# Kernel tuning notes

Hardware: AMD Instinct MI355X
Metric: run time of the kernel (lower is better)

The kernel has to match this reference:

```python
import jax, jax.numpy as jnp
import numpy as np

N = 50000      # nodes
E = 800000     # edges
IN = 30        # atom features
H = 8          # attention heads
D = 32         # per-head out feats
G = 512        # graphs in batch
HID = 128      # predictor hidden
TASKS = 1
ALPHA = 0.2    # LeakyReLU slope
BN_EPS = 1e-5


def setup_inputs() -> dict:
    key = jax.random.key(0)
    ks = jax.random.split(key, 20)
    f = lambda k, shp: (jax.random.normal(k, shp, dtype=jnp.float32) * 0.1)
    return {
        'x': jax.random.normal(ks[0], (N, IN), dtype=jnp.float32),
        'src': jax.random.randint(ks[1], (E,), 0, N, dtype=jnp.int32),
        'dst': jax.random.randint(ks[2], (E,), 0, N, dtype=jnp.int32),
        'graph_ids': jnp.sort(jax.random.randint(ks[3], (N,), 0, G, dtype=jnp.int32)),
        # GAT layer 1 (in=30 -> 8 heads x 32, flatten + ELU, residual projection)
        'W1': f(ks[4], (IN, H * D)),
        'al1': f(ks[5], (H, D)),
        'ar1': f(ks[6], (H, D)),
        'b1': jnp.zeros((H * D,), jnp.float32),
        'resW1': f(ks[7], (IN, H * D)),
        # GAT layer 2 (in=256 -> 8 heads x 32, mean over heads, identity residual)
        'W2': f(ks[8], (H * D, H * D)),
        'al2': f(ks[9], (H, D)),
        'ar2': f(ks[10], (H, D)),
        'b2': jnp.zeros((H * D,), jnp.float32),
        # WeightedSumAndMax readout gate
        'Ww': f(ks[11], (D, 1)),
        'bw': jnp.zeros((1,), jnp.float32),
        # MLP predictor: Linear -> ReLU -> BatchNorm(eval) -> Linear
        'Wp1': f(ks[12], (2 * D, HID)),
        'bp1': jnp.zeros((HID,), jnp.float32),
        'gamma': jnp.ones((HID,), jnp.float32),
        'beta': jnp.zeros((HID,), jnp.float32),
        'rm': jnp.zeros((HID,), jnp.float32),
        'rv': jnp.ones((HID,), jnp.float32),
        'Wp2': f(ks[13], (HID, TASKS)),
        'bp2': jnp.zeros((TASKS,), jnp.float32),
    }


def _gat_layer(h, src, dst, W, al, ar, b):
    # h: [N, F_in] -> out: [N, H, D]
    n = h.shape[0]
    feat = (h @ W).reshape(n, H, D)                    # projected features
    el = jnp.sum(feat * al, axis=-1)                   # [N, H]
    er = jnp.sum(feat * ar, axis=-1)                   # [N, H]
    e = el[src] + er[dst]                              # [E, H]
    e = jnp.where(e > 0, e, ALPHA * e)                 # LeakyReLU
    m = jax.ops.segment_max(e, dst, num_segments=n)    # segment-softmax max
    m = jnp.where(jnp.isfinite(m), m, 0.0)             # guard empty segments
    ex = jnp.exp(e - m[dst])                           # [E, H]
    s = jax.ops.segment_sum(ex, dst, num_segments=n)   # [N, H]
    a = ex / jnp.maximum(s[dst], 1e-9)                 # normalized attention
    msg = a[:, :, None] * feat[src]                    # [E, H, D]
    out = jax.ops.segment_sum(msg, dst, num_segments=n)
    return out + b.reshape(1, H, D)


def reference(x, src, dst, graph_ids, W1, al1, ar1, b1, resW1,
              W2, al2, ar2, b2, Ww, bw, Wp1, bp1, gamma, beta, rm, rv, Wp2, bp2):
    # Layer 1: residual projection (in_feats != H*D), flatten heads, ELU
    h1 = _gat_layer(x, src, dst, W1, al1, ar1, b1)
    h1 = h1 + (x @ resW1).reshape(N, H, D)
    h1 = jax.nn.elu(h1.reshape(N, H * D))
    # Layer 2: identity residual (in_feats == H*D), mean over heads, no activation
    h2 = _gat_layer(h1, src, dst, W2, al2, ar2, b2)
    h2 = h2 + h1.reshape(N, H, D)
    h2 = jnp.mean(h2, axis=1)                          # [N, D]
    # WeightedSumAndMax readout
    w = jax.nn.sigmoid(h2 @ Ww + bw)                   # [N, 1]
    gsum = jax.ops.segment_sum(w * h2, graph_ids, num_segments=G)
    gmax = jax.ops.segment_max(h2, graph_ids, num_segments=G)
    gmax = jnp.where(jnp.isfinite(gmax), gmax, 0.0)
    g = jnp.concatenate([gsum, gmax], axis=-1)         # [G, 2D]
    # MLP predictor (eval-mode BatchNorm)
    p = jax.nn.relu(g @ Wp1 + bp1)
    p = (p - rm) / jnp.sqrt(rv + BN_EPS) * gamma + beta
    return p @ Wp2 + bp2                               # [G, TASKS]
```

## Files before the change

kernel.cpp:

```cpp
#include <hip/hip_runtime.h>
#include <math.h>

#define NN 50000
#define EE 800000
#define IN_F 30
#define NH 8
#define DH 32
#define HD 256
#define NG 512
#define NHID 128
#define ALPHA 0.2f

#define SCAN_B 256
#define SCAN_NB ((NN + SCAN_B - 1)/SCAN_B)

typedef unsigned short u16;

__device__ __forceinline__ u16 f2bf(float f){
  unsigned u = __float_as_uint(f);
  u = u + 0x7FFFu + ((u >> 16) & 1u);
  return (u16)(u >> 16);
}
__device__ __forceinline__ float bf2f(u16 b){
  return __uint_as_float(((unsigned)b) << 16);
}
__device__ __forceinline__ float4 bf4_to_f4(ushort4 v){
  float4 r; r.x=bf2f(v.x); r.y=bf2f(v.y); r.z=bf2f(v.z); r.w=bf2f(v.w); return r;
}

__global__ void k_init(int* counts, int* gcounts){
  int i = blockIdx.x*blockDim.x + threadIdx.x;
  if(i < NN) counts[i] = 0;
  if(i < NG) gcounts[i] = 0;
}

__global__ void k_hist(const int* __restrict__ dst, int* counts){
  int i = blockIdx.x*blockDim.x + threadIdx.x;
  if(i < EE) atomicAdd(&counts[dst[i]], 1);
}

__global__ void k_ghist(const int* __restrict__ gid, int* gcounts){
  int i = blockIdx.x*blockDim.x + threadIdx.x;
  if(i < NN) atomicAdd(&gcounts[gid[i]], 1);
}

__global__ void k_gscan(const int* __restrict__ gcounts, int* __restrict__ gstart){
  __shared__ int sd[NG];
  int t = threadIdx.x;
  int v = gcounts[t];
  sd[t]=v; __syncthreads();
  for(int off=1; off<NG; off<<=1){
    int u = (t>=off)? sd[t-off] : 0;
    __syncthreads();
    sd[t] += u;
    __syncthreads();
  }
  gstart[t] = sd[t]-v;
}

__global__ void k_scan_partial(const int* __restrict__ counts, int* __restrict__ bsums){
  __shared__ int sd[SCAN_B];
  int b = blockIdx.x, t = threadIdx.x;
  int idx = b*SCAN_B + t;
  sd[t] = (idx<NN)? counts[idx] : 0;
  __syncthreads();
  for(int off=SCAN_B/2; off>0; off>>=1){
    if(t<off) sd[t] += sd[t+off];
    __syncthreads();
  }
  if(t==0) bsums[b] = sd[0];
}

__global__ void k_scan_bsums(int* bsums){
  __shared__ int sd[SCAN_B];
  int t = threadIdx.x;
  int v = (t<SCAN_NB)? bsums[t] : 0;
  sd[t]=v; __syncthreads();
  for(int off=1; off<SCAN_B; off<<=1){
    int u = (t>=off)? sd[t-off] : 0;
    __syncthreads();
    sd[t] += u;
    __syncthreads();
  }
  if(t<SCAN_NB) bsums[t] = sd[t]-v;
}

__global__ void k_scan_final(const int* __restrict__ counts, const int* __restrict__ bsums,
                             int* __restrict__ start, int* __restrict__ cursor){
  __shared__ int sd[SCAN_B];
  int b = blockIdx.x, t = threadIdx.x;
  int idx = b*SCAN_B + t;
  int v = (idx<NN)? counts[idx] : 0;
  sd[t]=v; __syncthreads();
  for(int off=1; off<SCAN_B; off<<=1){
    int u = (t>=off)? sd[t-off] : 0;
    __syncthreads();
    sd[t] += u;
    __syncthreads();
  }
  int ex = sd[t]-v + bsums[b];
  if(idx<NN){ start[idx]=ex; cursor[idx]=ex; }
}

__global__ void k_scatter(const int* __restrict__ dst, const int* __restrict__ src,
                          int* cursor, int* __restrict__ csr_src){
  int i = blockIdx.x*blockDim.x + threadIdx.x;
  if(i<EE){ int p = atomicAdd(&cursor[dst[i]],1); csr_src[p]=src[i]; }
}

#define TM1 16
__global__ void k_proj1(const float* __restrict__ x, const float* __restrict__ W1,
                        u16* __restrict__ feat16){
  __shared__ float xs[TM1][IN_F];
  int n0 = blockIdx.x*TM1;
  int t = threadIdx.x;
  for(int i=t;i<TM1*IN_F;i+=256){
    int m=i/IN_F, k=i-m*IN_F;
    xs[m][k] = x[(size_t)(n0+m)*IN_F+k];
  }
  __syncthreads();
  int jq = (t & 63) << 2;
  int m0 = t >> 6;
  float4 acc[4];
  #pragma unroll
  for(int r=0;r<4;r++){ acc[r].x=0.f; acc[r].y=0.f; acc[r].z=0.f; acc[r].w=0.f; }
  for(int k=0;k<IN_F;k++){
    float4 w = *(const float4*)&W1[k*HD + jq];
    #pragma unroll
    for(int r=0;r<4;r++){
      float xv = xs[m0 + (r<<2)][k];
      acc[r].x += xv*w.x; acc[r].y += xv*w.y; acc[r].z += xv*w.z; acc[r].w += xv*w.w;
    }
  }
  #pragma unroll
  for(int r=0;r<4;r++){
    int n = n0 + m0 + (r<<2);
    ushort4 o; o.x=f2bf(acc[r].x); o.y=f2bf(acc[r].y); o.z=f2bf(acc[r].z); o.w=f2bf(acc[r].w);
    *(ushort4*)&feat16[(size_t)n*HD + jq] = o;
  }
}

#define BM 64
#define BN 64
#define BK 16
#define LDP (BM+4)
__global__ void k_proj2(const float* __restrict__ X, const float* __restrict__ W,
                        u16* __restrict__ Y16){
  __shared__ float As[BK][LDP];
  __shared__ float Bs[BK][LDP];
  int t  = threadIdx.x;
  int tx = t & 15, ty = t >> 4;
  int n0 = blockIdx.x*BM;
  int c0 = blockIdx.y*BN;
  float acc[4][4];
  #pragma unroll
  for(int i=0;i<4;i++)
    #pragma unroll
    for(int j=0;j<4;j++) acc[i][j]=0.f;

  int am = t >> 2;
  int ak = (t & 3) << 2;
  int bk = t >> 4;
  int bn = (t & 15) << 2;

  for(int k0=0;k0<HD;k0+=BK){
    int n = n0 + am;
    float4 va = (n<NN) ? *(const float4*)&X[(size_t)n*HD + k0 + ak]
                       : make_float4(0.f,0.f,0.f,0.f);
    float4 vb = *(const float4*)&W[(size_t)(k0+bk)*HD + c0 + bn];
    __syncthreads();
    As[ak+0][am]=va.x; As[ak+1][am]=va.y; As[ak+2][am]=va.z; As[ak+3][am]=va.w;
    *(float4*)&Bs[bk][bn] = vb;
    __syncthreads();
    #pragma unroll
    for(int k=0;k<BK;k++){
      float4 a = *(const float4*)&As[k][ty<<2];
      float4 b = *(const float4*)&Bs[k][tx<<2];
      acc[0][0]+=a.x*b.x; acc[0][1]+=a.x*b.y; acc[0][2]+=a.x*b.z; acc[0][3]+=a.x*b.w;
      acc[1][0]+=a.y*b.x; acc[1][1]+=a.y*b.y; acc[1][2]+=a.y*b.z; acc[1][3]+=a.y*b.w;
      acc[2][0]+=a.z*b.x; acc[2][1]+=a.z*b.y; acc[2][2]+=a.z*b.z; acc[2][3]+=a.z*b.w;
      acc[3][0]+=a.w*b.x; acc[3][1]+=a.w*b.y; acc[3][2]+=a.w*b.z; acc[3][3]+=a.w*b.w;
    }
  }
  #pragma unroll
  for(int i=0;i<4;i++){
    int n = n0 + (ty<<2) + i;
    if(n<NN){
      ushort4 o; o.x=f2bf(acc[i][0]); o.y=f2bf(acc[i][1]); o.z=f2bf(acc[i][2]); o.w=f2bf(acc[i][3]);
      *(ushort4*)&Y16[(size_t)n*HD + c0 + (tx<<2)] = o;
    }
  }
}

__global__ void k_elr(const u16* __restrict__ feat16, const float* __restrict__ al,
                      const float* __restrict__ ar, float* __restrict__ el,
                      float* __restrict__ er){
  int i = blockIdx.x*blockDim.x + threadIdx.x;
  if(i >= NN*NH) return;
  int h = i & 7;
  const ushort4* f4 = (const ushort4*)(feat16 + (size_t)i*DH);
  const float4* a4 = (const float4*)(al + h*DH);
  const float4* b4 = (const float4*)(ar + h*DH);
  float ea=0.f, eb=0.f;
  #pragma unroll
  for(int q=0;q<8;q++){
    float4 f=bf4_to_f4(f4[q]); float4 a=a4[q], b=b4[q];
    ea += f.x*a.x + f.y*a.y + f.z*a.z + f.w*a.w;
    eb += f.x*b.x + f.y*b.y + f.z*b.z + f.w*b.w;
  }
  el[i]=ea; er[i]=eb;
}

__device__ __forceinline__ void gat_agg2(int n, int lane,
    const u16* __restrict__ feat16, const float* __restrict__ el,
    const float* __restrict__ er, const int* __restrict__ start,
    const int* __restrict__ counts, const int* __restrict__ csr_src,
    float* A){
  int half = lane >> 5;
  int l = lane & 31;
  int h = l >> 2;
  int col8 = l << 3;
  float erh = er[n*NH + h];
  int st = start[n], cnt = counts[n];
  float s = 0.f;
  #pragma unroll
  for(int j=0;j<8;j++) A[j]=0.f;
  for(int c=0; c<cnt; c+=64){
    int nrem = cnt - c;
    int lim = nrem < 64 ? nrem : 64;
    int myIdx = csr_src[st + c + (lane < lim ? lane : lim-1)];
    #pragma unroll 4
    for(int k=0; k<lim; k+=2){
      int sel = k + half;
      int sidx = __shfl(myIdx, sel, 64);
      float e = el[(size_t)sidx*NH + h] + erh;
      e = (e>0.f)? e : ALPHA*e;
      float w = (sel < lim) ? __expf(e) : 0.f;
      uint4 rv = *(const uint4*)&feat16[(size_t)sidx*HD + col8];
      float f0 = __uint_as_float(rv.x << 16);
      float f1 = __uint_as_float(rv.x & 0xffff0000u);
      float f2 = __uint_as_float(rv.y << 16);
      float f3 = __uint_as_float(rv.y & 0xffff0000u);
      float f4 = __uint_as_float(rv.z << 16);
      float f5 = __uint_as_float(rv.z & 0xffff0000u);
      float f6 = __uint_as_float(rv.w << 16);
      float f7 = __uint_as_float(rv.w & 0xffff0000u);
      s += w;
      A[0]+=w*f0; A[1]+=w*f1; A[2]+=w*f2; A[3]+=w*f3;
      A[4]+=w*f4; A[5]+=w*f5; A[6]+=w*f6; A[7]+=w*f7;
    }
  }
  s += __shfl_xor(s, 32, 64);
  #pragma unroll
  for(int j=0;j<8;j++) A[j] += __shfl_xor(A[j], 32, 64);
  float inv = 1.f/fmaxf(s, 1e-9f);
  #pragma unroll
  for(int j=0;j<8;j++) A[j] *= inv;
}

__global__ void k_gat1(const u16* __restrict__ feat16, const float* __restrict__ el,
    const float* __restrict__ er, const int* __restrict__ start,
    const int* __restrict__ counts, const int* __restrict__ csr_src,
    const float* __restrict__ x,
    const float* __restrict__ resW1, const float* __restrict__ b1,
    float* __restrict__ h1){
  int n = blockIdx.x*4 + (threadIdx.x>>6);
  int lane = threadIdx.x & 63;
  if(n>=NN) return;
  float A[8];
  gat_agg2(n,lane,feat16,el,er,start,counts,csr_src,A);
  int half = lane>>5, l = lane&31;
  int col8 = l<<3;
  float r[8];
  #pragma unroll
  for(int j=0;j<8;j++) r[j]=0.f;
  const float* xrow = x + (size_t)n*IN_F;
  int kb = half*15;
  #pragma unroll
  for(int k=0;k<15;k++){
    float xv = xrow[kb+k];
    const float4 w0 = *(const float4*)&resW1[(kb+k)*HD + col8];
    const float4 w1 = *(const float4*)&resW1[(kb+k)*HD + col8 + 4];
    r[0]+=xv*w0.x; r[1]+=xv*w0.y; r[2]+=xv*w0.z; r[3]+=xv*w0.w;
    r[4]+=xv*w1.x; r[5]+=xv*w1.y; r[6]+=xv*w1.z; r[7]+=xv*w1.w;
  }
  #pragma unroll
  for(int j=0;j<8;j++) r[j] += __shfl_xor(r[j], 32, 64);
  if(half==0){
    const float4 b0 = *(const float4*)&b1[col8];
    const float4 b4 = *(const float4*)&b1[col8+4];
    float4 o0, o1; float v;
    v = A[0]+r[0]+b0.x; o0.x = (v>0.f)? v : expf(v)-1.f;
    v = A[1]+r[1]+b0.y; o0.y = (v>0.f)? v : expf(v)-1.f;
    v = A[2]+r[2]+b0.z; o0.z = (v>0.f)? v : expf(v)-1.f;
    v = A[3]+r[3]+b0.w; o0.w = (v>0.f)? v : expf(v)-1.f;
    v = A[4]+r[4]+b4.x; o1.x = (v>0.f)? v : expf(v)-1.f;
    v = A[5]+r[5]+b4.y; o1.y = (v>0.f)? v : expf(v)-1.f;
    v = A[6]+r[6]+b4.z; o1.z = (v>0.f)? v : expf(v)-1.f;
    v = A[7]+r[7]+b4.w; o1.w = (v>0.f)? v : expf(v)-1.f;
    *(float4*)&h1[(size_t)n*HD + col8]     = o0;
    *(float4*)&h1[(size_t)n*HD + col8 + 4] = o1;
  }
}

__global__ void k_gat2(const u16* __restrict__ feat16, const float* __restrict__ el,
    const float* __restrict__ er, const int* __restrict__ start,
    const int* __restrict__ counts, const int* __restrict__ csr_src,
    const float* __restrict__ h1,
    const float* __restrict__ b2, float* __restrict__ h2){
  int n = blockIdx.x*4 + (threadIdx.x>>6);
  int lane = threadIdx.x & 63;
  if(n>=NN) return;
  float A[8];
  gat_agg2(n,lane,feat16,el,er,start,counts,csr_src,A);
  int l = lane&31;
  int col8 = l<<3;
  if(lane<32){
    const float4 b0 = *(const float4*)&b2[col8];
    const float4 b4 = *(const float4*)&b2[col8+4];
    const float4 h0 = *(const float4*)&h1[(size_t)n*HD + col8];
    const float4 h4 = *(const float4*)&h1[(size_t)n*HD + col8 + 4];
    float t[8];
    t[0]=A[0]+b0.x+h0.x; t[1]=A[1]+b0.y+h0.y; t[2]=A[2]+b0.z+h0.z; t[3]=A[3]+b0.w+h0.w;
    t[4]=A[4]+b4.x+h4.x; t[5]=A[5]+b4.y+h4.y; t[6]=A[6]+b4.z+h4.z; t[7]=A[7]+b4.w+h4.w;
    #pragma unroll
    for(int off=4; off<32; off<<=1){
      #pragma unroll
      for(int j=0;j<8;j++) t[j] += __shfl_xor(t[j], off, 64);
    }
    if(l<4){
      float4 o0, o1;
      o0.x=t[0]*0.125f; o0.y=t[1]*0.125f; o0.z=t[2]*0.125f; o0.w=t[3]*0.125f;
      o1.x=t[4]*0.125f; o1.y=t[5]*0.125f; o1.z=t[6]*0.125f; o1.w=t[7]*0.125f;
      *(float4*)&h2[(size_t)n*DH + (l<<3)]     = o0;
      *(float4*)&h2[(size_t)n*DH + (l<<3) + 4] = o1;
    }
  }
}

__global__ void k_readout(const float* __restrict__ h2, const float* __restrict__ Ww,
    const float* __restrict__ bw, const int* __restrict__ gstart,
    const int* __restrict__ gcounts, float* __restrict__ gsum,
    float* __restrict__ gmaxf){
  __shared__ float ssum[8][DH];
  __shared__ float smax[8][DH];
  int g = blockIdx.x;
  int t = threadIdx.x;
  int half = (t & 63) >> 5;
  int wid = t >> 6;
  int l = t & 31;
  int rg = wid*2 + half;
  int s = gstart[g], cnt = gcounts[g];
  float w_d = Ww[l];
  float bw0 = bw[0];
  float sum = 0.f, mx = -INFINITY;
  for(int r = rg; r < cnt; r += 8){
    float v = h2[(size_t)(s+r)*DH + l];
    float p = v*w_d;
    p += __shfl_xor(p,1,64); p += __shfl_xor(p,2,64); p += __shfl_xor(p,4,64);
    p += __shfl_xor(p,8,64); p += __shfl_xor(p,16,64);
    float wg = 1.f/(1.f+__expf(-(p+bw0)));
    sum += wg*v;
    mx = fmaxf(mx, v);
  }
  ssum[rg][l] = sum;
  smax[rg][l] = mx;
  __syncthreads();
  if(t < DH){
    float a = 0.f, m = -INFINITY;
    #pragma unroll
    for(int r=0;r<8;r++){ a += ssum[r][t]; m = fmaxf(m, smax[r][t]); }
    gsum[g*DH+t]  = a;
    gmaxf[g*DH+t] = isfinite(m)? m : 0.f;
  }
}

__global__ void k_mlp(const float* __restrict__ gsum, const float* __restrict__ gmaxf,
    const float* __restrict__ Wp1, const float* __restrict__ bp1,
    const float* __restrict__ gamma, const float* __restrict__ beta,
    const float* __restrict__ rm, const float* __restrict__ rv,
    const float* __restrict__ Wp2, const float* __restrict__ bp2,
    float* __restrict__ out){
  __shared__ float gs[2*DH];
  __shared__ float red[NHID];
  int g = blockIdx.x, t = threadIdx.x;
  if(t < DH) gs[t] = gsum[g*DH + t];
  else if(t < 2*DH) gs[t] = gmaxf[g*DH + (t-DH)];
  __syncthreads();
  float acc = bp1[t];
  #pragma unroll
  for(int k=0;k<2*DH;k++) acc += gs[k]*Wp1[k*NHID + t];
  acc = fmaxf(acc, 0.f);
  acc = (acc - rm[t])*rsqrtf(rv[t]+1e-5f)*gamma[t] + beta[t];
  red[t] = acc*Wp2[t];
  __syncthreads();
  for(int off=NHID/2; off>0; off>>=1){
    if(t<off) red[t] += red[t+off];
    __syncthreads();
  }
  if(t==0) out[g] = red[0] + bp2[0];
}

extern "C" void kernel_launch(void* const* d_in, const int* in_sizes, int n_in,
                              void* d_out, int out_size, void* d_ws, size_t ws_size,
                              hipStream_t stream){
  const float* x    = (const float*)d_in[0];
  const int*   src  = (const int*)  d_in[1];
  const int*   dst  = (const int*)  d_in[2];
  const int*   gid  = (const int*)  d_in[3];
  const float* W1   = (const float*)d_in[4];
  const float* al1  = (const float*)d_in[5];
  const float* ar1  = (const float*)d_in[6];
  const float* b1   = (const float*)d_in[7];
  const float* resW1= (const float*)d_in[8];
  const float* W2   = (const float*)d_in[9];
  const float* al2  = (const float*)d_in[10];
  const float* ar2  = (const float*)d_in[11];
  const float* b2   = (const float*)d_in[12];
  const float* Ww   = (const float*)d_in[13];
  const float* bw   = (const float*)d_in[14];
  const float* Wp1  = (const float*)d_in[15];
  const float* bp1  = (const float*)d_in[16];
  const float* gamma= (const float*)d_in[17];
  const float* beta = (const float*)d_in[18];
  const float* rm   = (const float*)d_in[19];
  const float* rv   = (const float*)d_in[20];
  const float* Wp2  = (const float*)d_in[21];
  const float* bp2  = (const float*)d_in[22];
  float* out = (float*)d_out;

  char* w = (char*)d_ws;
  u16*      feat16 = (u16*)w;      w += (size_t)NN*HD*2;
  float*    h1     = (float*)w;    w += (size_t)NN*HD*4;
  float*    el     = (float*)w;    w += (size_t)NN*NH*4;
  float*    er     = (float*)w;    w += (size_t)NN*NH*4;
  float*    h2     = (float*)w;    w += (size_t)NN*DH*4;
  float*    gsum   = (float*)w;    w += (size_t)NG*DH*4;
  float*    gmaxf  = (float*)w;    w += (size_t)NG*DH*4;
  int*      counts = (int*)w;      w += (size_t)NN*4;
  int*      start  = (int*)w;      w += (size_t)NN*4;
  int*      cursor = (int*)w;      w += (size_t)NN*4;
  int*      bsums  = (int*)w;      w += (size_t)SCAN_NB*4;
  int*      gcounts= (int*)w;      w += (size_t)NG*4;
  int*      gstart = (int*)w;      w += (size_t)NG*4;
  int*      csr_src= (int*)w;      w += (size_t)EE*4;

  hipLaunchKernelGGL(k_init,         dim3((NN+255)/256),       dim3(256),    0, stream, counts, gcounts);
  hipLaunchKernelGGL(k_hist,         dim3((EE+255)/256),       dim3(256),    0, stream, dst, counts);
  hipLaunchKernelGGL(k_ghist,        dim3((NN+255)/256),       dim3(256),    0, stream, gid, gcounts);
  hipLaunchKernelGGL(k_gscan,        dim3(1),                  dim3(NG),     0, stream, gcounts, gstart);
  hipLaunchKernelGGL(k_scan_partial, dim3(SCAN_NB),            dim3(SCAN_B), 0, stream, counts, bsums);
  hipLaunchKernelGGL(k_scan_bsums,   dim3(1),                  dim3(SCAN_B), 0, stream, bsums);
  hipLaunchKernelGGL(k_scan_final,   dim3(SCAN_NB),            dim3(SCAN_B), 0, stream, counts, bsums, start, cursor);
  hipLaunchKernelGGL(k_scatter,      dim3((EE+255)/256),       dim3(256),    0, stream, dst, src, cursor, csr_src);
  hipLaunchKernelGGL(k_proj1,        dim3(NN/TM1),             dim3(256),    0, stream, x, W1, feat16);
  hipLaunchKernelGGL(k_elr,          dim3((NN*NH+255)/256),    dim3(256),    0, stream, feat16, al1, ar1, el, er);
  hipLaunchKernelGGL(k_gat1,         dim3((NN+3)/4),           dim3(256),    0, stream, feat16, el, er, start, counts, csr_src, x, resW1, b1, h1);
  hipLaunchKernelGGL(k_proj2,        dim3((NN+BM-1)/BM, HD/BN), dim3(256),   0, stream, h1, W2, feat16);
  hipLaunchKernelGGL(k_elr,          dim3((NN*NH+255)/256),    dim3(256),    0, stream, feat16, al2, ar2, el, er);
  hipLaunchKernelGGL(k_gat2,         dim3((NN+3)/4),           dim3(256),    0, stream, feat16, el, er, start, counts, csr_src, h1, b2, h2);
  hipLaunchKernelGGL(k_readout,      dim3(NG),                 dim3(256),    0, stream, h2, Ww, bw, gstart, gcounts, gsum, gmaxf);
  hipLaunchKernelGGL(k_mlp,          dim3(NG),                 dim3(NHID),   0, stream, gsum, gmaxf, Wp1, bp1, gamma, beta, rm, rv, Wp2, bp2, out);
}
```

Measured before the change: 562.4 us.

## Use bf16 MFMA for layer-2 projection, store h1 in bf16, degree-sort nodes

```diff
diff --git a/kernel.cpp b/kernel.cpp
--- a/kernel.cpp
+++ b/kernel.cpp
@@ -13,8 +13,11 @@
 
 #define SCAN_B 256
 #define SCAN_NB ((NN + SCAN_B - 1)/SCAN_B)
+#define DB 64
 
 typedef unsigned short u16;
+typedef __attribute__((ext_vector_type(8))) short bf16x8;
+typedef __attribute__((ext_vector_type(4))) float f32x4;
 
 __device__ __forceinline__ u16 f2bf(float f){
   unsigned u = __float_as_uint(f);
@@ -28,10 +31,11 @@
   float4 r; r.x=bf2f(v.x); r.y=bf2f(v.y); r.z=bf2f(v.z); r.w=bf2f(v.w); return r;
 }
 
-__global__ void k_init(int* counts, int* gcounts){
+__global__ void k_init(int* counts, int* gcounts, int* dcnt){
   int i = blockIdx.x*blockDim.x + threadIdx.x;
   if(i < NN) counts[i] = 0;
   if(i < NG) gcounts[i] = 0;
+  if(i < DB) dcnt[i] = 0;
 }
 
 __global__ void k_hist(const int* __restrict__ dst, int* counts){
@@ -108,6 +112,36 @@
   if(i<EE){ int p = atomicAdd(&cursor[dst[i]],1); csr_src[p]=src[i]; }
 }
 
+__global__ void k_dhist(const int* __restrict__ counts, int* dcnt){
+  int i = blockIdx.x*blockDim.x + threadIdx.x;
+  if(i<NN){ int b = min(counts[i], DB-1); atomicAdd(&dcnt[b],1); }
+}
+__global__ void k_dscan(const int* __restrict__ dcnt, int* __restrict__ dcur){
+  __shared__ int sd[DB];
+  int t = threadIdx.x;
+  int v = dcnt[t];
+  sd[t]=v; __syncthreads();
+  for(int off=1; off<DB; off<<=1){
+    int u = (t>=off)? sd[t-off] : 0;
+    __syncthreads();
+    sd[t] += u;
+    __syncthreads();
+  }
+  dcur[t] = sd[t]-v;
+}
+__global__ void k_dscatter(const int* __restrict__ counts, int* dcur,
+                           int* __restrict__ node_order){
+  int i = blockIdx.x*blockDim.x + threadIdx.x;
+  if(i<NN){ int b = min(counts[i], DB-1); int p = atomicAdd(&dcur[b],1); node_order[p]=i; }
+}
+
+__global__ void k_w2t(const float* __restrict__ W2, u16* __restrict__ W2T){
+  int i = blockIdx.x*blockDim.x + threadIdx.x;
+  if(i >= HD*HD) return;
+  int n = i >> 8, k = i & 255;
+  W2T[i] = f2bf(W2[k*HD + n]);
+}
+
 #define TM1 16
 __global__ void k_proj1(const float* __restrict__ x, const float* __restrict__ W1,
                         u16* __restrict__ feat16){
@@ -140,54 +174,34 @@
   }
 }
 
-#define BM 64
-#define BN 64
-#define BK 16
-#define LDP (BM+4)
-__global__ void k_proj2(const float* __restrict__ X, const float* __restrict__ W,
-                        u16* __restrict__ Y16){
-  __shared__ float As[BK][LDP];
-  __shared__ float Bs[BK][LDP];
-  int t  = threadIdx.x;
-  int tx = t & 15, ty = t >> 4;
-  int n0 = blockIdx.x*BM;
-  int c0 = blockIdx.y*BN;
-  float acc[4][4];
-  #pragma unroll
-  for(int i=0;i<4;i++)
+__global__ void k_proj2m(const u16* __restrict__ h1b, const u16* __restrict__ W2T,
+                         u16* __restrict__ Y16){
+  int t = threadIdx.x;
+  int wave = t>>6, lane = t&63;
+  int m0 = blockIdx.x*64 + wave*16;
+  int c0 = blockIdx.y*64;
+  int lm = lane & 15, lq = lane >> 4;
+  int arow = m0 + lm; if(arow >= NN) arow = NN-1;
+  const u16* Aptr = h1b + (size_t)arow*HD + lq*8;
+  f32x4 acc[4];
+  #pragma unroll
+  for(int ct=0;ct<4;ct++) acc[ct] = (f32x4){0.f,0.f,0.f,0.f};
+  #pragma unroll
+  for(int k0=0;k0<HD;k0+=32){
+    bf16x8 a = *(const bf16x8*)(Aptr + k0);
     #pragma unroll
-    for(int j=0;j<4;j++) acc[i][j]=0.f;
-
-  int am = t >> 2;
-  int ak = (t & 3) << 2;
-  int bk = t >> 4;
-  int bn = (t & 15) << 2;
-
-  for(int k0=0;k0<HD;k0+=BK){
-    int n = n0 + am;
-    float4 va = (n<NN) ? *(const float4*)&X[(size_t)n*HD + k0 + ak]
-                       : make_float4(0.f,0.f,0.f,0.f);
-    float4 vb = *(const float4*)&W[(size_t)(k0+bk)*HD + c0 + bn];
-    __syncthreads();
-    As[ak+0][am]=va.x; As[ak+1][am]=va.y; As[ak+2][am]=va.z; As[ak+3][am]=va.w;
-    *(float4*)&Bs[bk][bn] = vb;
-    __syncthreads();
+    for(int ct=0;ct<4;ct++){
+      bf16x8 b = *(const bf16x8*)(W2T + (size_t)(c0 + ct*16 + lm)*HD + k0 + lq*8);
+      acc[ct] = __builtin_amdgcn_mfma_f32_16x16x32_bf16(a, b, acc[ct], 0, 0, 0);
+    }
+  }
+  int orow0 = m0 + lq*4;
+  #pragma unroll
+  for(int ct=0;ct<4;ct++){
     #pragma unroll
-    for(int k=0;k<BK;k++){
-      float4 a = *(const float4*)&As[k][ty<<2];
-      float4 b = *(const float4*)&Bs[k][tx<<2];
-      acc[0][0]+=a.x*b.x; acc[0][1]+=a.x*b.y; acc[0][2]+=a.x*b.z; acc[0][3]+=a.x*b.w;
-      acc[1][0]+=a.y*b.x; acc[1][1]+=a.y*b.y; acc[1][2]+=a.y*b.z; acc[1][3]+=a.y*b.w;
-      acc[2][0]+=a.z*b.x; acc[2][1]+=a.z*b.y; acc[2][2]+=a.z*b.z; acc[2][3]+=a.z*b.w;
-      acc[3][0]+=a.w*b.x; acc[3][1]+=a.w*b.y; acc[3][2]+=a.w*b.z; acc[3][3]+=a.w*b.w;
-    }
-  }
-  #pragma unroll
-  for(int i=0;i<4;i++){
-    int n = n0 + (ty<<2) + i;
-    if(n<NN){
-      ushort4 o; o.x=f2bf(acc[i][0]); o.y=f2bf(acc[i][1]); o.z=f2bf(acc[i][2]); o.w=f2bf(acc[i][3]);
-      *(ushort4*)&Y16[(size_t)n*HD + c0 + (tx<<2)] = o;
+    for(int r=0;r<4;r++){
+      int n = orow0 + r;
+      if(n < NN) Y16[(size_t)n*HD + c0 + ct*16 + lm] = f2bf(acc[ct][r]);
     }
   }
 }
@@ -261,12 +275,11 @@
 __global__ void k_gat1(const u16* __restrict__ feat16, const float* __restrict__ el,
     const float* __restrict__ er, const int* __restrict__ start,
     const int* __restrict__ counts, const int* __restrict__ csr_src,
-    const float* __restrict__ x,
+    const int* __restrict__ node_order, const float* __restrict__ x,
     const float* __restrict__ resW1, const float* __restrict__ b1,
-    float* __restrict__ h1){
-  int n = blockIdx.x*4 + (threadIdx.x>>6);
+    u16* __restrict__ h1b){
+  int n = node_order[blockIdx.x*4 + (threadIdx.x>>6)];
   int lane = threadIdx.x & 63;
-  if(n>=NN) return;
   float A[8];
   gat_agg2(n,lane,feat16,el,er,start,counts,csr_src,A);
   int half = lane>>5, l = lane&31;
@@ -289,28 +302,27 @@
   if(half==0){
     const float4 b0 = *(const float4*)&b1[col8];
     const float4 b4 = *(const float4*)&b1[col8+4];
-    float4 o0, o1; float v;
-    v = A[0]+r[0]+b0.x; o0.x = (v>0.f)? v : expf(v)-1.f;
-    v = A[1]+r[1]+b0.y; o0.y = (v>0.f)? v : expf(v)-1.f;
-    v = A[2]+r[2]+b0.z; o0.z = (v>0.f)? v : expf(v)-1.f;
-    v = A[3]+r[3]+b0.w; o0.w = (v>0.f)? v : expf(v)-1.f;
-    v = A[4]+r[4]+b4.x; o1.x = (v>0.f)? v : expf(v)-1.f;
-    v = A[5]+r[5]+b4.y; o1.y = (v>0.f)? v : expf(v)-1.f;
-    v = A[6]+r[6]+b4.z; o1.z = (v>0.f)? v : expf(v)-1.f;
-    v = A[7]+r[7]+b4.w; o1.w = (v>0.f)? v : expf(v)-1.f;
-    *(float4*)&h1[(size_t)n*HD + col8]     = o0;
-    *(float4*)&h1[(size_t)n*HD + col8 + 4] = o1;
+    float v; ushort4 q0, q1;
+    v = A[0]+r[0]+b0.x; q0.x = f2bf((v>0.f)? v : expf(v)-1.f);
+    v = A[1]+r[1]+b0.y; q0.y = f2bf((v>0.f)? v : expf(v)-1.f);
+    v = A[2]+r[2]+b0.z; q0.z = f2bf((v>0.f)? v : expf(v)-1.f);
+    v = A[3]+r[3]+b0.w; q0.w = f2bf((v>0.f)? v : expf(v)-1.f);
+    v = A[4]+r[4]+b4.x; q1.x = f2bf((v>0.f)? v : expf(v)-1.f);
+    v = A[5]+r[5]+b4.y; q1.y = f2bf((v>0.f)? v : expf(v)-1.f);
+    v = A[6]+r[6]+b4.z; q1.z = f2bf((v>0.f)? v : expf(v)-1.f);
+    v = A[7]+r[7]+b4.w; q1.w = f2bf((v>0.f)? v : expf(v)-1.f);
+    *(ushort4*)&h1b[(size_t)n*HD + col8]     = q0;
+    *(ushort4*)&h1b[(size_t)n*HD + col8 + 4] = q1;
   }
 }
 
 __global__ void k_gat2(const u16* __restrict__ feat16, const float* __restrict__ el,
     const float* __restrict__ er, const int* __restrict__ start,
     const int* __restrict__ counts, const int* __restrict__ csr_src,
-    const float* __restrict__ h1,
+    const int* __restrict__ node_order, const u16* __restrict__ h1b,
     const float* __restrict__ b2, float* __restrict__ h2){
-  int n = blockIdx.x*4 + (threadIdx.x>>6);
+  int n = node_order[blockIdx.x*4 + (threadIdx.x>>6)];
   int lane = threadIdx.x & 63;
-  if(n>=NN) return;
   float A[8];
   gat_agg2(n,lane,feat16,el,er,start,counts,csr_src,A);
   int l = lane&31;
@@ -318,8 +330,8 @@
   if(lane<32){
     const float4 b0 = *(const float4*)&b2[col8];
     const float4 b4 = *(const float4*)&b2[col8+4];
-    const float4 h0 = *(const float4*)&h1[(size_t)n*HD + col8];
-    const float4 h4 = *(const float4*)&h1[(size_t)n*HD + col8 + 4];
+    float4 h0 = bf4_to_f4(*(const ushort4*)&h1b[(size_t)n*HD + col8]);
+    float4 h4 = bf4_to_f4(*(const ushort4*)&h1b[(size_t)n*HD + col8 + 4]);
     float t[8];
     t[0]=A[0]+b0.x+h0.x; t[1]=A[1]+b0.y+h0.y; t[2]=A[2]+b0.z+h0.z; t[3]=A[3]+b0.w+h0.w;
     t[4]=A[4]+b4.x+h4.x; t[5]=A[5]+b4.y+h4.y; t[6]=A[6]+b4.z+h4.z; t[7]=A[7]+b4.w+h4.w;
@@ -431,7 +443,8 @@
 
   char* w = (char*)d_ws;
   u16*      feat16 = (u16*)w;      w += (size_t)NN*HD*2;
-  float*    h1     = (float*)w;    w += (size_t)NN*HD*4;
+  u16*      h1b    = (u16*)w;      w += (size_t)NN*HD*2;
+  u16*      W2T    = (u16*)w;      w += (size_t)HD*HD*2;
   float*    el     = (float*)w;    w += (size_t)NN*NH*4;
   float*    er     = (float*)w;    w += (size_t)NN*NH*4;
   float*    h2     = (float*)w;    w += (size_t)NN*DH*4;
@@ -443,9 +456,12 @@
   int*      bsums  = (int*)w;      w += (size_t)SCAN_NB*4;
   int*      gcounts= (int*)w;      w += (size_t)NG*4;
   int*      gstart = (int*)w;      w += (size_t)NG*4;
+  int*      dcnt   = (int*)w;      w += (size_t)DB*4;
+  int*      dcur   = (int*)w;      w += (size_t)DB*4;
+  int*      node_order=(int*)w;    w += (size_t)NN*4;
   int*      csr_src= (int*)w;      w += (size_t)EE*4;
 
-  hipLaunchKernelGGL(k_init,         dim3((NN+255)/256),       dim3(256),    0, stream, counts, gcounts);
+  hipLaunchKernelGGL(k_init,         dim3((NN+255)/256),       dim3(256),    0, stream, counts, gcounts, dcnt);
   hipLaunchKernelGGL(k_hist,         dim3((EE+255)/256),       dim3(256),    0, stream, dst, counts);
   hipLaunchKernelGGL(k_ghist,        dim3((NN+255)/256),       dim3(256),    0, stream, gid, gcounts);
   hipLaunchKernelGGL(k_gscan,        dim3(1),                  dim3(NG),     0, stream, gcounts, gstart);
@@ -453,12 +469,16 @@
   hipLaunchKernelGGL(k_scan_bsums,   dim3(1),                  dim3(SCAN_B), 0, stream, bsums);
   hipLaunchKernelGGL(k_scan_final,   dim3(SCAN_NB),            dim3(SCAN_B), 0, stream, counts, bsums, start, cursor);
   hipLaunchKernelGGL(k_scatter,      dim3((EE+255)/256),       dim3(256),    0, stream, dst, src, cursor, csr_src);
+  hipLaunchKernelGGL(k_dhist,        dim3((NN+255)/256),       dim3(256),    0, stream, counts, dcnt);
+  hipLaunchKernelGGL(k_dscan,        dim3(1),                  dim3(DB),     0, stream, dcnt, dcur);
+  hipLaunchKernelGGL(k_dscatter,     dim3((NN+255)/256),       dim3(256),    0, stream, counts, dcur, node_order);
+  hipLaunchKernelGGL(k_w2t,          dim3((HD*HD+255)/256),    dim3(256),    0, stream, W2, W2T);
   hipLaunchKernelGGL(k_proj1,        dim3(NN/TM1),             dim3(256),    0, stream, x, W1, feat16);
   hipLaunchKernelGGL(k_elr,          dim3((NN*NH+255)/256),    dim3(256),    0, stream, feat16, al1, ar1, el, er);
-  hipLaunchKernelGGL(k_gat1,         dim3((NN+3)/4),           dim3(256),    0, stream, feat16, el, er, start, counts, csr_src, x, resW1, b1, h1);
-  hipLaunchKernelGGL(k_proj2,        dim3((NN+BM-1)/BM, HD/BN), dim3(256),   0, stream, h1, W2, feat16);
+  hipLaunchKernelGGL(k_gat1,         dim3(NN/4),               dim3(256),    0, stream, feat16, el, er, start, counts, csr_src, node_order, x, resW1, b1, h1b);
+  hipLaunchKernelGGL(k_proj2m,       dim3((NN+63)/64, HD/64),  dim3(256),    0, stream, h1b, W2T, feat16);
   hipLaunchKernelGGL(k_elr,          dim3((NN*NH+255)/256),    dim3(256),    0, stream, feat16, al2, ar2, el, er);
-  hipLaunchKernelGGL(k_gat2,         dim3((NN+3)/4),           dim3(256),    0, stream, feat16, el, er, start, counts, csr_src, h1, b2, h2);
+  hipLaunchKernelGGL(k_gat2,         dim3(NN/4),               dim3(256),    0, stream, feat16, el, er, start, counts, csr_src, node_order, h1b, b2, h2);
   hipLaunchKernelGGL(k_readout,      dim3(NG),                 dim3(256),    0, stream, h2, Ww, bw, gstart, gcounts, gsum, gmaxf);
   hipLaunchKernelGGL(k_mlp,          dim3(NG),                 dim3(NHID),   0, stream, gsum, gmaxf, Wp1, bp1, gamma, beta, rm, rv, Wp2, bp2, out);
 }
```

Result: slower. 820.2 us (+45.9%).
